# Kernel optimization log

Hardware: AMD Instinct MI355X
Metric: run time of the kernel (lower is better)

Reference implementation:

```python
import jax, jax.numpy as jnp
import numpy as np

B, T, C, H = 2, 2048, 1024, 16
HD = C // H
MAX_WAVELENGTH = 10000.0


def apply_rope(x, positions):
    # x: [B, H, T, HD], positions: [T]
    fraction = 2.0 * jnp.arange(HD // 2, dtype=jnp.float32) / HD
    timescale = MAX_WAVELENGTH ** fraction  # [HD//2]
    sinusoid = positions[:, None] / timescale[None, :]  # [T, HD//2]
    sin = jnp.sin(sinusoid)
    cos = jnp.cos(sinusoid)
    first, second = jnp.split(x, 2, axis=-1)
    out = jnp.concatenate(
        [first * cos - second * sin, second * cos + first * sin], axis=-1
    )
    return out.astype(x.dtype)


def setup_inputs() -> dict:
    key = jax.random.key(0)
    k1, k2, k3 = jax.random.split(key, 3)
    x = jax.random.normal(k1, (B, T, C), dtype=jnp.float32)
    w_attn = jax.random.normal(k2, (C, 3 * C), dtype=jnp.float32) * 0.02
    b_attn = jnp.zeros((3 * C,), dtype=jnp.float32)
    w_proj = jax.random.normal(k3, (C, C), dtype=jnp.float32) * 0.02
    b_proj = jnp.zeros((C,), dtype=jnp.float32)
    return {"x": x, "w_attn": w_attn, "b_attn": b_attn,
            "w_proj": w_proj, "b_proj": b_proj}


def reference(x, w_attn, b_attn, w_proj, b_proj):
    b, t, c = x.shape
    qkv = x @ w_attn + b_attn  # [B, T, 3C]
    q, k, v = jnp.split(qkv, 3, axis=-1)
    q = q.reshape(b, t, H, HD).transpose(0, 2, 1, 3)  # [B, H, T, HD]
    k = k.reshape(b, t, H, HD).transpose(0, 2, 1, 3)
    v = v.reshape(b, t, H, HD).transpose(0, 2, 1, 3)
    positions = jnp.arange(t, dtype=x.dtype)
    q = apply_rope(q, positions)
    k = apply_rope(k, positions)
    att = jnp.einsum('bhqd,bhkd->bhqk', q, k) * (1.0 / jnp.sqrt(HD))
    causal = jnp.tril(jnp.ones((t, t), dtype=bool))
    att = jnp.where(causal, att, jnp.finfo(att.dtype).min)
    att = jax.nn.softmax(att, axis=-1)
    y = jnp.einsum('bhqk,bhkd->bhqd', att, v)
    y = y.transpose(0, 2, 1, 3).reshape(b, t, c)
    return y @ w_proj + b_proj
```

## Files before the change

kernel.cpp:

```cpp
#include <hip/hip_runtime.h>
#include <hip/hip_bf16.h>


typedef __attribute__((ext_vector_type(8))) short short8;
typedef __attribute__((ext_vector_type(4))) float floatx4;

__device__ __forceinline__ unsigned short f2bf(float f) {
    union { float f; unsigned int u; } v; v.f = f;
    unsigned int r = v.u + 0x7FFFu + ((v.u >> 16) & 1u);
    return (unsigned short)(r >> 16);
}

__device__ __forceinline__ unsigned int pk2bf(float a, float b) {
    union { float f; unsigned int u; } ua, ub;
    ua.f = a; ub.f = b;
    return __builtin_amdgcn_perm(ub.u + 0x8000u, ua.u + 0x8000u, 0x07060302u);
}

__device__ __forceinline__ unsigned int cvtpk(float a, float b) {
    unsigned int r;
    asm("v_cvt_pk_bf16_f32 %0, %1, %2" : "=v"(r) : "v"(a), "v"(b));
    return r;
}

__device__ __forceinline__ void gld16(const void* g, void* l) {
    __builtin_amdgcn_global_load_lds(
        (const __attribute__((address_space(1))) unsigned int*)g,
        (__attribute__((address_space(3))) unsigned int*)l, 16, 0, 0);
}

__device__ __forceinline__ void transpose_body(
    const float* __restrict__ in, unsigned short* __restrict__ out,
    int R, int NC, int bx, int by, int tid,
    unsigned short (*tile)[68]) {
    int r0 = by * 64, c0 = bx * 64;
    int c4 = (tid & 15) * 4, rr = tid >> 4;
#pragma unroll
    for (int i = 0; i < 4; i++) {
        int row = rr + i * 16;
        float4 v = *(const float4*)&in[(size_t)(r0 + row) * NC + c0 + c4];
        ushort4 o;
        o.x = f2bf(v.x); o.y = f2bf(v.y); o.z = f2bf(v.z); o.w = f2bf(v.w);
        *(ushort4*)&tile[row][c4] = o;
    }
    __syncthreads();
    int col = tid & 63, rr2 = tid >> 6;
#pragma unroll
    for (int i = 0; i < 16; i++) {
        int orow = rr2 + i * 4;
        out[(size_t)(c0 + orow) * R + r0 + col] = tile[col][orow];
    }
}

__global__ __launch_bounds__(256) void prep(
    const float* __restrict__ x,
    const float* __restrict__ w_attn,
    const float* __restrict__ w_proj,
    unsigned short* __restrict__ x_bf,
    unsigned short* __restrict__ wTa,
    unsigned short* __restrict__ wTp,
    float2* __restrict__ tab) {
    __shared__ unsigned short tile[64][68];
    int bid = blockIdx.x;
    int tid = threadIdx.x;
    if (bid < 4096) {
        int i = bid * 256 + tid;
        float4 v = ((const float4*)x)[i];
        ushort4 o;
        o.x = f2bf(v.x); o.y = f2bf(v.y); o.z = f2bf(v.z); o.w = f2bf(v.w);
        ((ushort4*)x_bf)[i] = o;
    } else if (bid < 4864) {
        int t = bid - 4096;
        transpose_body(w_attn, wTa, 1024, 3072, t % 48, t / 48, tid, tile);
    } else if (bid < 5120) {
        int t = bid - 4864;
        transpose_body(w_proj, wTp, 1024, 1024, t & 15, t >> 4, tid, tile);
    } else {
        int i = (bid - 5120) * 256 + tid;
        int t = i >> 5, d = i & 31;
        float inv_ts = exp2f(-0.41524101186092036f * (float)d);
        float ang = (float)t * inv_ts;
        tab[i] = make_float2(sinf(ang), cosf(ang));
    }
}

__global__ __launch_bounds__(512) void gemm_qkv(
    const unsigned short* __restrict__ A,
    const unsigned short* __restrict__ BT,
    const float* __restrict__ bias,
    const float2* __restrict__ tab,
    unsigned short* __restrict__ qT,
    unsigned short* __restrict__ kT,
    unsigned short* __restrict__ vT) {
    __shared__ __align__(16) unsigned short smem[65536];
    int tid = threadIdx.x;
    int lane = tid & 63;
    int w = tid >> 6;
    int wx = w & 3, wy = w >> 2;
    int l16 = lane & 15, quad = lane >> 4;
    int lin = blockIdx.x;
    int m0 = (lin >> 3) * 128;
    int ng = lin & 7;
    int n0 = ng * 384;
    int x = l16 & 7;
    int lr = lane >> 3;
    int gc = (lane & 7) ^ lr;

    floatx4 acc[4][6];
#pragma unroll
    for (int mi = 0; mi < 4; mi++)
#pragma unroll
        for (int ni = 0; ni < 6; ni++)
            acc[mi][ni] = (floatx4){0.f, 0.f, 0.f, 0.f};

    auto stage = [&](int bsel, int k0) {
        unsigned short* as = smem + bsel * 32768;
        unsigned short* bs = as + 8192;
#pragma unroll
        for (int i = 0; i < 2; i++) {
            int seg = w * 2 + i;
            int row = seg * 8 + lr;
            gld16(A + (size_t)(m0 + row) * 1024 + k0 + gc * 8, &as[seg * 512]);
        }
#pragma unroll
        for (int i = 0; i < 6; i++) {
            int seg = w * 6 + i;
            int row = seg * 8 + lr;
            gld16(BT + (size_t)(n0 + row) * 1024 + k0 + gc * 8, &bs[seg * 512]);
        }
    };

    auto compute = [&](int bsel) {
        const unsigned short* as = smem + bsel * 32768;
        const unsigned short* bs = as + 8192;
#pragma unroll
        for (int kk = 0; kk < 2; kk++) {
            short8 af[4], bf[6];
#pragma unroll
            for (int mi = 0; mi < 4; mi++) {
                int r = wy * 64 + mi * 16 + l16;
                af[mi] = *(const short8*)&as[r * 64 + (((kk << 2) | quad) ^ x) * 8];
            }
#pragma unroll
            for (int ni = 0; ni < 6; ni++) {
                int r = wx * 96 + ni * 16 + l16;
                bf[ni] = *(const short8*)&bs[r * 64 + (((kk << 2) | quad) ^ x) * 8];
            }
#pragma unroll
            for (int mi = 0; mi < 4; mi++)
#pragma unroll
                for (int ni = 0; ni < 6; ni++)
                    acc[mi][ni] = __builtin_amdgcn_mfma_f32_16x16x32_bf16(
                        af[mi], bf[ni], acc[mi][ni], 0, 0, 0);
        }
    };

    stage(0, 0);
    int cur = 0;
    for (int k0 = 0; k0 < 1024; k0 += 64) {
        asm volatile("s_waitcnt vmcnt(0)" ::: "memory");
        __builtin_amdgcn_s_barrier();
        if (k0 < 960) stage(cur ^ 1, k0 + 64);
        compute(cur);
        cur ^= 1;
    }
    __syncthreads();

    int b = m0 >> 11;
    float bb[6];
#pragma unroll
    for (int ni = 0; ni < 6; ni++)
        bb[ni] = bias[n0 + wx * 96 + ni * 16 + l16];

    float* F = (float*)smem;
    unsigned short* U = smem + 16512;
    unsigned short* V = smem;

    for (int g = 0; g < 6; g++) {
        int col0 = n0 + g * 64;
        int region = col0 >> 10;
        if (region < 2) {
            unsigned short* qk = region ? kT : qT;
            float scale = region ? 1.0f : 0.18033688011112042f;
#pragma unroll
            for (int mi = 0; mi < 4; mi++)
#pragma unroll
                for (int ni = 0; ni < 6; ni++) {
                    int c = wx * 96 + ni * 16;
                    if ((c >> 6) == g) {
                        int dl = c - g * 64 + l16;
#pragma unroll
                        for (int r = 0; r < 4; r++) {
                            int row = wy * 64 + mi * 16 + quad * 4 + r;
                            F[dl * 129 + row] = acc[mi][ni][r] + bb[ni];
                        }
                    }
                }
            __syncthreads();
            {
                int tl = tid >> 2, sub = tid & 3;
                int t = (m0 & 2047) + tl;
                int d0 = sub * 8;
                unsigned int lo[4], hi[4];
#pragma unroll
                for (int j = 0; j < 8; j += 2) {
                    float o1[2], o2[2];
#pragma unroll
                    for (int e = 0; e < 2; e++) {
                        int d = d0 + j + e;
                        float v1 = F[d * 129 + tl];
                        float v2 = F[(d + 32) * 129 + tl];
                        float2 sc = tab[t * 32 + d];
                        o1[e] = (v1 * sc.y - v2 * sc.x) * scale;
                        o2[e] = (v2 * sc.y + v1 * sc.x) * scale;
                    }
                    lo[j >> 1] = (unsigned int)f2bf(o1[0]) |
                                 ((unsigned int)f2bf(o1[1]) << 16);
                    hi[j >> 1] = (unsigned int)f2bf(o2[0]) |
                                 ((unsigned int)f2bf(o2[1]) << 16);
                }
                *(uint2*)&U[tl * 72 + d0]          = make_uint2(lo[0], lo[1]);
                *(uint2*)&U[tl * 72 + d0 + 4]      = make_uint2(lo[2], lo[3]);
                *(uint2*)&U[tl * 72 + 32 + d0]     = make_uint2(hi[0], hi[1]);
                *(uint2*)&U[tl * 72 + 32 + d0 + 4] = make_uint2(hi[2], hi[3]);
            }
            __syncthreads();
            {
                int h = (col0 & 1023) >> 6;
                unsigned short* ob = qk + (size_t)(b * 16 + h) * 2048 * 64;
                int rr = tid >> 3;
                int c8 = tid & 7;
#pragma unroll
                for (int p = 0; p < 2; p++) {
                    int row = rr + p * 64;
                    int t = (m0 & 2047) + row;
                    short8 val = *(const short8*)&U[row * 72 + c8 * 8];
                    *(short8*)&ob[(size_t)t * 64 + c8 * 8] = val;
                }
            }
            __syncthreads();
        } else {
#pragma unroll
            for (int mi = 0; mi < 4; mi++)
#pragma unroll
                for (int ni = 0; ni < 6; ni++) {
                    int c = wx * 96 + ni * 16;
                    if ((c >> 6) == g) {
                        int dl = c - g * 64 + l16;
                        int t_base = wy * 64 + mi * 16 + quad * 4;
                        float bv = bb[ni];
                        uint2 pk;
                        pk.x = pk2bf(acc[mi][ni][0] + bv, acc[mi][ni][1] + bv);
                        pk.y = pk2bf(acc[mi][ni][2] + bv, acc[mi][ni][3] + bv);
                        int e = dl * 128 + (t_base ^ ((dl & 15) << 3));
                        *(uint2*)&V[e] = pk;
                    }
                }
            __syncthreads();
            {
                int d_r = tid >> 3;
                int c8 = tid & 7;
                int cv = (col0 - 2048) + d_r;
                int hh = cv >> 6, dd = cv & 63;
                int fofs = (d_r & 15) << 3;
                size_t vbase = ((size_t)(b * 16 + hh) * 64 + dd) * 2048 + (m0 & 2047);
#pragma unroll
                for (int p = 0; p < 2; p++) {
                    int tc = c8 * 8 + p * 64;
                    short8 val = *(const short8*)&V[d_r * 128 + (tc ^ fofs)];
                    *(short8*)&vT[vbase + tc] = val;
                }
            }
            __syncthreads();
        }
    }
}

__global__ __launch_bounds__(256) void gemm_proj(
    const unsigned short* __restrict__ A,
    const unsigned short* __restrict__ BT,
    const float* __restrict__ bias,
    float* __restrict__ out) {
    __shared__ __align__(16) unsigned short smem[24576];
    int lane = threadIdx.x & 63;
    int w = threadIdx.x >> 6;
    int wx = w & 1, wy = w >> 1;
    int l16 = lane & 15, quad = lane >> 4;
    int lin = blockIdx.x;
    int swz = (lin & 7) * 64 + (lin >> 3);
    int m0 = (swz >> 4) * 128;
    int n0 = (swz & 15) * 64;
    int x = l16 & 7;
    int lr = lane >> 3;
    int gc = (lane & 7) ^ lr;

    floatx4 acc[4][2];
#pragma unroll
    for (int mi = 0; mi < 4; mi++)
#pragma unroll
        for (int ni = 0; ni < 2; ni++)
            acc[mi][ni] = (floatx4){0.f, 0.f, 0.f, 0.f};

    auto stage = [&](int bsel, int k0) {
        unsigned short* as = smem + bsel * 12288;
        unsigned short* bs = as + 8192;
#pragma unroll
        for (int i = 0; i < 6; i++) {
            int seg = w * 6 + i;
            if (seg < 16) {
                int row = seg * 8 + lr;
                gld16(A + (size_t)(m0 + row) * 1024 + k0 + gc * 8, &as[seg * 512]);
            } else {
                int s2 = seg - 16;
                int row = s2 * 8 + lr;
                gld16(BT + (size_t)(n0 + row) * 1024 + k0 + gc * 8, &bs[s2 * 512]);
            }
        }
    };

    auto compute = [&](int bsel) {
        const unsigned short* as = smem + bsel * 12288;
        const unsigned short* bs = as + 8192;
#pragma unroll
        for (int kk = 0; kk < 2; kk++) {
            short8 af[4], bf[2];
#pragma unroll
            for (int mi = 0; mi < 4; mi++) {
                int r = wy * 64 + mi * 16 + l16;
                af[mi] = *(const short8*)&as[r * 64 + (((kk << 2) | quad) ^ x) * 8];
            }
#pragma unroll
            for (int ni = 0; ni < 2; ni++) {
                int r = wx * 32 + ni * 16 + l16;
                bf[ni] = *(const short8*)&bs[r * 64 + (((kk << 2) | quad) ^ x) * 8];
            }
#pragma unroll
            for (int mi = 0; mi < 4; mi++)
#pragma unroll
                for (int ni = 0; ni < 2; ni++)
                    acc[mi][ni] = __builtin_amdgcn_mfma_f32_16x16x32_bf16(
                        af[mi], bf[ni], acc[mi][ni], 0, 0, 0);
        }
    };

    stage(0, 0);
    int cur = 0;
    for (int k0 = 0; k0 < 1024; k0 += 64) {
        asm volatile("s_waitcnt vmcnt(0)" ::: "memory");
        __builtin_amdgcn_s_barrier();
        if (k0 < 960) stage(cur ^ 1, k0 + 64);
        compute(cur);
        cur ^= 1;
    }

#pragma unroll
    for (int mi = 0; mi < 4; mi++)
#pragma unroll
        for (int ni = 0; ni < 2; ni++) {
            int row = m0 + wy * 64 + mi * 16 + quad * 4;
            int col = n0 + wx * 32 + ni * 16 + l16;
            float bv = bias[col];
#pragma unroll
            for (int r = 0; r < 4; r++)
                out[(size_t)(row + r) * 1024 + col] = acc[mi][ni][r] + bv;
        }
}

__global__ __launch_bounds__(256) void attn5(
    const unsigned short* __restrict__ qT,
    const unsigned short* __restrict__ kT,
    const unsigned short* __restrict__ vT,
    unsigned short* __restrict__ y) {
    __shared__ __align__(16) unsigned short kbuf[2][64 * 64];
    __shared__ __align__(16) unsigned short vbuf[2][64 * 64];
    __shared__ __align__(16) unsigned short pl[4][16 * 72];
    int lane = threadIdx.x & 63;
    int w = threadIdx.x >> 6;
    int l16 = lane & 15, quad = lane >> 4;
    int blk = blockIdx.x;
    int t = 31 - (blk >> 5);
    int bh = blk & 31;
    int b = bh >> 4, h = bh & 15;
    int q0 = t * 64 + w * 16;
    const unsigned short* qp = qT + (size_t)bh * 2048 * 64;
    unsigned short* plw = pl[w];
    int x = l16 & 7;

    short8 qf0 = *(const short8*)(qp + (size_t)(q0 + l16) * 64 + quad * 8);
    short8 qf1 = *(const short8*)(qp + (size_t)(q0 + l16) * 64 + 32 + quad * 8);

    short8 ones;
#pragma unroll
    for (int j = 0; j < 8; j++) ones[j] = (short)0x3F80;

    floatx4 acc[4];
#pragma unroll
    for (int ni = 0; ni < 4; ni++) acc[ni] = (floatx4){0.f, 0.f, 0.f, 0.f};
    floatx4 accl = (floatx4){0.f, 0.f, 0.f, 0.f};

    int lr8 = lane >> 3, l8 = lane & 7;
    const unsigned short* sp[4];
    unsigned short* ld0[4];
    int gstep;
    if (w < 2) {
        const unsigned short* kp = kT + (size_t)bh * 2048 * 64;
#pragma unroll
        for (int i = 0; i < 4; i++) {
            int seg = w * 4 + i;
            int row = seg * 8 + lr8;
            int c = l8 ^ (row & 7);
            sp[i] = kp + (size_t)row * 64 + c * 8;
            ld0[i] = &kbuf[0][seg * 512];
        }
        gstep = 4096;
    } else {
        const unsigned short* vp = vT + (size_t)bh * 64 * 2048;
#pragma unroll
        for (int i = 0; i < 4; i++) {
            int s = (w - 2) * 4 + i;
            int d = s * 8 + lr8;
            int c = l8 ^ (d & 7);
            sp[i] = vp + (size_t)d * 2048 + c * 8;
            ld0[i] = &vbuf[0][s * 512];
        }
        gstep = 64;
    }

    auto stage = [&](int bi) {
#pragma unroll
        for (int i = 0; i < 4; i++) {
            gld16(sp[i], ld0[i] + bi * 4096);
            sp[i] += gstep;
        }
    };

    int L = t + 1;
    int query = q0 + l16;
    stage(0);
    int cur = 0;
    for (int it = 0; it < L; it++) {
        asm volatile("s_waitcnt vmcnt(0)" ::: "memory");
        __builtin_amdgcn_s_barrier();
        if (it + 1 < L) stage(cur ^ 1);
        const unsigned short* kb = kbuf[cur];
        const unsigned short* vb = vbuf[cur];
        bool diag = (it == t);
        floatx4 s4[4];
        __builtin_amdgcn_s_setprio(1);
#pragma unroll
        for (int c = 0; c < 4; c++) {
            int r = c * 16 + l16;
            short8 kf0 = *(const short8*)&kb[r * 64 + ((quad) ^ x) * 8];
            short8 kf1 = *(const short8*)&kb[r * 64 + ((quad | 4) ^ x) * 8];
            floatx4 z = (floatx4){0.f, 0.f, 0.f, 0.f};
            z = __builtin_amdgcn_mfma_f32_16x16x32_bf16(kf0, qf0, z, 0, 0, 0);
            z = __builtin_amdgcn_mfma_f32_16x16x32_bf16(kf1, qf1, z, 0, 0, 0);
            s4[c] = z;
        }
        __builtin_amdgcn_s_setprio(0);
        int j0 = it * 64;
#pragma unroll
        for (int c = 0; c < 4; c++) {
            float p[4];
#pragma unroll
            for (int r = 0; r < 4; r++) {
                float e = __builtin_amdgcn_exp2f(s4[c][r]);
                if (diag) {
                    int key = j0 + c * 16 + quad * 4 + r;
                    e = (key <= query) ? e : 0.f;
                }
                p[r] = e;
            }
            uint2 pk;
            pk.x = cvtpk(p[0], p[1]);
            pk.y = cvtpk(p[2], p[3]);
            *(uint2*)&plw[l16 * 72 + c * 16 + quad * 4] = pk;
        }
        short8 pa0 = *(const short8*)&plw[l16 * 72 + quad * 8];
        short8 pa1 = *(const short8*)&plw[l16 * 72 + 32 + quad * 8];
        __builtin_amdgcn_s_setprio(1);
        accl = __builtin_amdgcn_mfma_f32_16x16x32_bf16(pa0, ones, accl, 0, 0, 0);
        accl = __builtin_amdgcn_mfma_f32_16x16x32_bf16(pa1, ones, accl, 0, 0, 0);
#pragma unroll
        for (int ni = 0; ni < 4; ni++) {
            int d = ni * 16 + l16;
            short8 vf0 = *(const short8*)&vb[d * 64 + ((quad) ^ x) * 8];
            short8 vf1 = *(const short8*)&vb[d * 64 + ((quad | 4) ^ x) * 8];
            acc[ni] = __builtin_amdgcn_mfma_f32_16x16x32_bf16(pa0, vf0, acc[ni], 0, 0, 0);
            acc[ni] = __builtin_amdgcn_mfma_f32_16x16x32_bf16(pa1, vf1, acc[ni], 0, 0, 0);
        }
        __builtin_amdgcn_s_setprio(0);
        cur ^= 1;
    }

    float inv[4];
#pragma unroll
    for (int r = 0; r < 4; r++) inv[r] = 1.f / accl[r];
#pragma unroll
    for (int ni = 0; ni < 4; ni++)
#pragma unroll
        for (int r = 0; r < 4; r++) {
            int tr = q0 + quad * 4 + r;
            y[((size_t)(b * 2048 + tr)) * 1024 + h * 64 + ni * 16 + l16] =
                f2bf(acc[ni][r] * inv[r]);
        }
}

extern "C" void kernel_launch(void* const* d_in, const int* in_sizes, int n_in,
                              void* d_out, int out_size, void* d_ws, size_t ws_size,
                              hipStream_t stream) {
    const float* x      = (const float*)d_in[0];
    const float* w_attn = (const float*)d_in[1];
    const float* b_attn = (const float*)d_in[2];
    const float* w_proj = (const float*)d_in[3];
    const float* b_proj = (const float*)d_in[4];
    float* out = (float*)d_out;

    char* ws = (char*)d_ws;
    unsigned short* x_bf = (unsigned short*)ws;
    unsigned short* wTa  = (unsigned short*)(ws + (8ull << 20));
    unsigned short* wTp  = (unsigned short*)(ws + (14ull << 20));
    unsigned short* qTb  = (unsigned short*)(ws + (16ull << 20));
    unsigned short* kTb  = (unsigned short*)(ws + (24ull << 20));
    unsigned short* vTb  = (unsigned short*)(ws + (32ull << 20));
    float2*         tab  = (float2*)(ws + (40ull << 20));
    unsigned short* y_bf = x_bf;

    prep<<<5376, 256, 0, stream>>>(x, w_attn, w_proj, x_bf, wTa, wTp, tab);
    gemm_qkv<<<256, 512, 0, stream>>>(x_bf, wTa, b_attn, tab, qTb, kTb, vTb);
    attn5<<<1024, 256, 0, stream>>>(qTb, kTb, vTb, y_bf);
    gemm_proj<<<512, 256, 0, stream>>>(y_bf, wTp, b_proj, out);
}
```

Measured before the change: 168.3 us.

## Double attention query tile per block and vectorize transpose stores

The attention kernel now processes 128 queries per block (32 per wave, two 16-row groups), so each staged K/V tile feeds twice as many MFMAs and total K/V global traffic is halved. The grid shrinks from 1024 to 512 blocks, and the last two key tiles get causal masking instead of only the diagonal one. Separately, the prep transpose writes 16-byte vectors per thread instead of scalar 2-byte stores. The cost is more accumulator registers, fewer blocks for load balancing, and a bit of wasted work on the masked tiles.

```diff
diff --git a/kernel.cpp b/kernel.cpp
--- a/kernel.cpp
+++ b/kernel.cpp
@@ -44,11 +44,14 @@
         *(ushort4*)&tile[row][c4] = o;
     }
     __syncthreads();
-    int col = tid & 63, rr2 = tid >> 6;
-#pragma unroll
-    for (int i = 0; i < 16; i++) {
-        int orow = rr2 + i * 4;
-        out[(size_t)(c0 + orow) * R + r0 + col] = tile[col][orow];
+    int s = tid & 7, oc0 = tid >> 3;
+#pragma unroll
+    for (int p = 0; p < 2; p++) {
+        int oc = oc0 + p * 32;
+        short8 tmp;
+#pragma unroll
+        for (int e = 0; e < 8; e++) tmp[e] = (short)tile[s * 8 + e][oc];
+        *(short8*)&out[(size_t)(c0 + oc) * R + r0 + s * 8] = tmp;
     }
 }
 
@@ -366,7 +369,7 @@
         }
 }
 
-__global__ __launch_bounds__(256) void attn5(
+__global__ __launch_bounds__(256) void attn6(
     const unsigned short* __restrict__ qT,
     const unsigned short* __restrict__ kT,
     const unsigned short* __restrict__ vT,
@@ -378,25 +381,33 @@
     int w = threadIdx.x >> 6;
     int l16 = lane & 15, quad = lane >> 4;
     int blk = blockIdx.x;
-    int t = 31 - (blk >> 5);
+    int jq = 15 - (blk >> 5);
     int bh = blk & 31;
     int b = bh >> 4, h = bh & 15;
-    int q0 = t * 64 + w * 16;
+    int q0 = jq * 128 + w * 32;
     const unsigned short* qp = qT + (size_t)bh * 2048 * 64;
     unsigned short* plw = pl[w];
     int x = l16 & 7;
 
-    short8 qf0 = *(const short8*)(qp + (size_t)(q0 + l16) * 64 + quad * 8);
-    short8 qf1 = *(const short8*)(qp + (size_t)(q0 + l16) * 64 + 32 + quad * 8);
+    short8 qf[2][2];
+#pragma unroll
+    for (int g = 0; g < 2; g++) {
+        qf[g][0] = *(const short8*)(qp + (size_t)(q0 + g * 16 + l16) * 64 + quad * 8);
+        qf[g][1] = *(const short8*)(qp + (size_t)(q0 + g * 16 + l16) * 64 + 32 + quad * 8);
+    }
 
     short8 ones;
 #pragma unroll
     for (int j = 0; j < 8; j++) ones[j] = (short)0x3F80;
 
-    floatx4 acc[4];
-#pragma unroll
-    for (int ni = 0; ni < 4; ni++) acc[ni] = (floatx4){0.f, 0.f, 0.f, 0.f};
-    floatx4 accl = (floatx4){0.f, 0.f, 0.f, 0.f};
+    floatx4 acc[2][4];
+#pragma unroll
+    for (int g = 0; g < 2; g++)
+#pragma unroll
+        for (int ni = 0; ni < 4; ni++) acc[g][ni] = (floatx4){0.f, 0.f, 0.f, 0.f};
+    floatx4 accl[2];
+    accl[0] = (floatx4){0.f, 0.f, 0.f, 0.f};
+    accl[1] = (floatx4){0.f, 0.f, 0.f, 0.f};
 
     int lr8 = lane >> 3, l8 = lane & 7;
     const unsigned short* sp[4];
@@ -434,8 +445,7 @@
         }
     };
 
-    int L = t + 1;
-    int query = q0 + l16;
+    int L = 2 * jq + 2;
     stage(0);
     int cur = 0;
     for (int it = 0; it < L; it++) {
@@ -444,66 +454,84 @@
         if (it + 1 < L) stage(cur ^ 1);
         const unsigned short* kb = kbuf[cur];
         const unsigned short* vb = vbuf[cur];
-        bool diag = (it == t);
-        floatx4 s4[4];
+        bool masked = (it >= 2 * jq);
+        floatx4 s4[2][4];
         __builtin_amdgcn_s_setprio(1);
 #pragma unroll
         for (int c = 0; c < 4; c++) {
             int r = c * 16 + l16;
             short8 kf0 = *(const short8*)&kb[r * 64 + ((quad) ^ x) * 8];
             short8 kf1 = *(const short8*)&kb[r * 64 + ((quad | 4) ^ x) * 8];
-            floatx4 z = (floatx4){0.f, 0.f, 0.f, 0.f};
-            z = __builtin_amdgcn_mfma_f32_16x16x32_bf16(kf0, qf0, z, 0, 0, 0);
-            z = __builtin_amdgcn_mfma_f32_16x16x32_bf16(kf1, qf1, z, 0, 0, 0);
-            s4[c] = z;
+#pragma unroll
+            for (int g = 0; g < 2; g++) {
+                floatx4 z = (floatx4){0.f, 0.f, 0.f, 0.f};
+                z = __builtin_amdgcn_mfma_f32_16x16x32_bf16(kf0, qf[g][0], z, 0, 0, 0);
+                z = __builtin_amdgcn_mfma_f32_16x16x32_bf16(kf1, qf[g][1], z, 0, 0, 0);
+                s4[g][c] = z;
+            }
         }
         __builtin_amdgcn_s_setprio(0);
         int j0 = it * 64;
-#pragma unroll
-        for (int c = 0; c < 4; c++) {
-            float p[4];
-#pragma unroll
-            for (int r = 0; r < 4; r++) {
-                float e = __builtin_amdgcn_exp2f(s4[c][r]);
-                if (diag) {
-                    int key = j0 + c * 16 + quad * 4 + r;
-                    e = (key <= query) ? e : 0.f;
+        short8 pa[2][2];
+#pragma unroll
+        for (int g = 0; g < 2; g++) {
+            int query = q0 + g * 16 + l16;
+#pragma unroll
+            for (int c = 0; c < 4; c++) {
+                float p[4];
+#pragma unroll
+                for (int r = 0; r < 4; r++) {
+                    float e = __builtin_amdgcn_exp2f(s4[g][c][r]);
+                    if (masked) {
+                        int key = j0 + c * 16 + quad * 4 + r;
+                        e = (key <= query) ? e : 0.f;
+                    }
+                    p[r] = e;
                 }
-                p[r] = e;
-            }
-            uint2 pk;
-            pk.x = cvtpk(p[0], p[1]);
-            pk.y = cvtpk(p[2], p[3]);
-            *(uint2*)&plw[l16 * 72 + c * 16 + quad * 4] = pk;
-        }
-        short8 pa0 = *(const short8*)&plw[l16 * 72 + quad * 8];
-        short8 pa1 = *(const short8*)&plw[l16 * 72 + 32 + quad * 8];
+                uint2 pk;
+                pk.x = cvtpk(p[0], p[1]);
+                pk.y = cvtpk(p[2], p[3]);
+                *(uint2*)&plw[l16 * 72 + c * 16 + quad * 4] = pk;
+            }
+            pa[g][0] = *(const short8*)&plw[l16 * 72 + quad * 8];
+            pa[g][1] = *(const short8*)&plw[l16 * 72 + 32 + quad * 8];
+        }
         __builtin_amdgcn_s_setprio(1);
-        accl = __builtin_amdgcn_mfma_f32_16x16x32_bf16(pa0, ones, accl, 0, 0, 0);
-        accl = __builtin_amdgcn_mfma_f32_16x16x32_bf16(pa1, ones, accl, 0, 0, 0);
+#pragma unroll
+        for (int g = 0; g < 2; g++) {
+            accl[g] = __builtin_amdgcn_mfma_f32_16x16x32_bf16(pa[g][0], ones, accl[g], 0, 0, 0);
+            accl[g] = __builtin_amdgcn_mfma_f32_16x16x32_bf16(pa[g][1], ones, accl[g], 0, 0, 0);
+        }
 #pragma unroll
         for (int ni = 0; ni < 4; ni++) {
             int d = ni * 16 + l16;
             short8 vf0 = *(const short8*)&vb[d * 64 + ((quad) ^ x) * 8];
             short8 vf1 = *(const short8*)&vb[d * 64 + ((quad | 4) ^ x) * 8];
-            acc[ni] = __builtin_amdgcn_mfma_f32_16x16x32_bf16(pa0, vf0, acc[ni], 0, 0, 0);
-            acc[ni] = __builtin_amdgcn_mfma_f32_16x16x32_bf16(pa1, vf1, acc[ni], 0, 0, 0);
+#pragma unroll
+            for (int g = 0; g < 2; g++) {
+                acc[g][ni] = __builtin_amdgcn_mfma_f32_16x16x32_bf16(pa[g][0], vf0, acc[g][ni], 0, 0, 0);
+                acc[g][ni] = __builtin_amdgcn_mfma_f32_16x16x32_bf16(pa[g][1], vf1, acc[g][ni], 0, 0, 0);
+            }
         }
         __builtin_amdgcn_s_setprio(0);
         cur ^= 1;
     }
 
-    float inv[4];
-#pragma unroll
-    for (int r = 0; r < 4; r++) inv[r] = 1.f / accl[r];
-#pragma unroll
-    for (int ni = 0; ni < 4; ni++)
-#pragma unroll
-        for (int r = 0; r < 4; r++) {
-            int tr = q0 + quad * 4 + r;
-            y[((size_t)(b * 2048 + tr)) * 1024 + h * 64 + ni * 16 + l16] =
-                f2bf(acc[ni][r] * inv[r]);
-        }
+    float inv[2][4];
+#pragma unroll
+    for (int g = 0; g < 2; g++)
+#pragma unroll
+        for (int r = 0; r < 4; r++) inv[g][r] = 1.f / accl[g][r];
+#pragma unroll
+    for (int g = 0; g < 2; g++)
+#pragma unroll
+        for (int ni = 0; ni < 4; ni++)
+#pragma unroll
+            for (int r = 0; r < 4; r++) {
+                int tr = q0 + g * 16 + quad * 4 + r;
+                y[((size_t)(b * 2048 + tr)) * 1024 + h * 64 + ni * 16 + l16] =
+                    f2bf(acc[g][ni][r] * inv[g][r]);
+            }
 }
 
 extern "C" void kernel_launch(void* const* d_in, const int* in_sizes, int n_in,
@@ -528,6 +556,6 @@
 
     prep<<<5376, 256, 0, stream>>>(x, w_attn, w_proj, x_bf, wTa, wTp, tab);
     gemm_qkv<<<256, 512, 0, stream>>>(x_bf, wTa, b_attn, tab, qTb, kTb, vTb);
-    attn5<<<1024, 256, 0, stream>>>(qTb, kTb, vTb, y_bf);
+    attn6<<<512, 256, 0, stream>>>(qTb, kTb, vTb, y_bf);
     gemm_proj<<<512, 256, 0, stream>>>(y_bf, wTp, b_proj, out);
 }
```

Measured after the change: 179.0 us. +6.3%, slower.
